# Kernel optimization log

Measured on AMD Instinct MI355X. Metric: run time of the kernel, lower is better.

## Reference

```python
import jax, jax.numpy as jnp
import numpy as np

B, C, H, W = 4, 512, 64, 64
R = 8
D = C // R  # inner channels = 64


def setup_inputs() -> dict:
    key = jax.random.key(0)
    k1, k2, k3 = jax.random.split(key, 3)
    x = jax.random.normal(k1, (B, C, H, W), dtype=jnp.float32)
    # 1x1 conv weights, stored as [out, in] (kernel spatial dims are 1)
    w_qkv = jax.random.normal(k2, (3 * D, C), dtype=jnp.float32) * (1.0 / np.sqrt(C))
    w_out = jax.random.normal(k3, (C, D), dtype=jnp.float32) * (1.0 / np.sqrt(D))
    # nn.Parameter(torch.zeros(1)) in the original; use nonzero so output != input
    scale = jnp.array([0.3], dtype=jnp.float32)
    return {"x": x, "w_qkv": w_qkv, "w_out": w_out, "scale": scale}


def reference(x, w_qkv, w_out, scale):
    b, c, h, w = x.shape
    hw = h * w
    # 1x1 conv == channel matmul
    t = jnp.einsum('oc,bchw->bohw', w_qkv, x)  # [B, 3D, H, W]
    d = t.shape[1] // 3
    key_ = t[:, :d].reshape(b, d, hw)      # chunk order: key, query, value
    query = t[:, d:2 * d].reshape(b, d, hw)
    value = t[:, 2 * d:].reshape(b, d, hw)
    # scores[b, k, q] = sum_d key[b,d,k] * query[b,d,q]
    scores = jnp.einsum('bdk,bdq->bkq', key_, query)  # [B, hw, hw]
    # NB: original uses Softmax(dim=1) -> normalize over the KEY axis
    attn = jax.nn.softmax(scores, axis=1)
    out = jnp.einsum('bdk,bkq->bdq', value, attn)     # [B, D, hw]
    out = out.reshape(b, d, h, w)
    out = jnp.einsum('oc,bchw->bohw', w_out, out)     # [B, C, H, W]
    return scale * out + x
```

## Files before the change

kernel.cpp:

```cpp
#include <hip/hip_runtime.h>
#include <hip/hip_bf16.h>
#include <string.h>

#define B_ 4
#define C_ 512
#define D_ 64
#define HW_ 4096
#define NCHUNK 4
#define KT_PER_CHUNK 16

typedef __attribute__((ext_vector_type(8))) short bf16x8;
typedef __attribute__((ext_vector_type(4))) float f32x4;

__device__ __forceinline__ unsigned short f2bf(float f) {
    unsigned int u = __builtin_bit_cast(unsigned int, f);
    u += 0x7fffu + ((u >> 16) & 1u);
    return (unsigned short)(u >> 16);
}

__device__ __forceinline__ unsigned int pack2bf(float lo, float hi) {
    __hip_bfloat162 h = __float22bfloat162_rn(float2{lo, hi});
    unsigned int r;
    memcpy(&r, &h, sizeof(r));
    return r;
}

#if __has_builtin(__builtin_amdgcn_exp2f)
#define EXP2(x) __builtin_amdgcn_exp2f(x)
#else
#define EXP2(x) __expf((x) * 0.6931471805599453f)
#endif

#define OFF_WQKV 0u
#define OFF_WOUT 196608u
#define OFF_PART 262144u
#define OFF_KT   17039360u
#define OFF_QT   19136512u
#define OFF_V    21233664u
#define OFF_ML   25427968u

__global__ __launch_bounds__(256) void k_convw(const float* __restrict__ wqkv,
                                               const float* __restrict__ wout,
                                               unsigned short* __restrict__ wq_b,
                                               unsigned short* __restrict__ wo_b) {
    int i = blockIdx.x * 256 + threadIdx.x;
    if (i < 192 * C_) wq_b[i] = f2bf(wqkv[i]);
    if (i < C_ * D_)  wo_b[i] = f2bf(wout[i]);
}

__global__ __launch_bounds__(256) void k_qkv(const float* __restrict__ x,
                                             const unsigned short* __restrict__ wq,
                                             unsigned short* __restrict__ kt,
                                             unsigned short* __restrict__ qt,
                                             unsigned short* __restrict__ v) {
    __shared__ float tile[64][33];
    __shared__ unsigned short xb[32][64];
    int pT = blockIdx.x, b = blockIdx.y;
    int tid = threadIdx.x, wid = tid >> 6, lane = tid & 63;
    int g = lane >> 4, r16 = lane & 15;
    int pp0 = pT * 32;
    int lp = tid & 31, lc = tid >> 5;
    int pl = tid >> 3, ch = tid & 7;

    float rx[8];
    auto gload = [&](int ct) {
        #pragma unroll
        for (int r = 0; r < 8; ++r)
            rx[r] = x[(size_t)(b * C_ + ct * 64 + lc * 8 + r) * HW_ + pp0 + lp];
    };

    f32x4 acc[3][2] = {};
    gload(0);
    for (int ct = 0; ct < 8; ++ct) {
        #pragma unroll
        for (int r = 0; r < 8; ++r) tile[lc * 8 + r][lp] = rx[r];
        __syncthreads();
        unsigned int pk[4];
        #pragma unroll
        for (int j = 0; j < 4; ++j)
            pk[j] = pack2bf(tile[ch * 8 + 2 * j][pl], tile[ch * 8 + 2 * j + 1][pl]);
        *(uint4*)(&xb[pl][0] + ((ch ^ (pl & 7)) << 3)) =
            make_uint4(pk[0], pk[1], pk[2], pk[3]);
        if (ct + 1 < 8) gload(ct + 1);
        __syncthreads();
        #pragma unroll
        for (int cs = 0; cs < 2; ++cs) {
            bf16x8 bb[2];
            #pragma unroll
            for (int ps = 0; ps < 2; ++ps) {
                int row = ps * 16 + r16;
                bb[ps] = *(const bf16x8*)(&xb[row][0] + (((cs * 4 + g) ^ (row & 7)) << 3));
            }
            #pragma unroll
            for (int ot = 0; ot < 3; ++ot) {
                bf16x8 a = *(const bf16x8*)(wq + (size_t)(wid * 48 + ot * 16 + r16) * C_
                                            + ct * 64 + cs * 32 + g * 8);
                #pragma unroll
                for (int ps = 0; ps < 2; ++ps)
                    acc[ot][ps] = __builtin_amdgcn_mfma_f32_16x16x32_bf16(a, bb[ps], acc[ot][ps], 0, 0, 0);
            }
        }
    }
    #pragma unroll
    for (int ot = 0; ot < 3; ++ot) {
        int obase = wid * 48 + ot * 16;
        int oT = obase >> 6;
        int dbase = (obase & 63) + 4 * g;
        #pragma unroll
        for (int ps = 0; ps < 2; ++ps) {
            int pp = pp0 + ps * 16 + r16;
            if (oT < 2) {
                unsigned short* dst = (oT == 0) ? kt : qt;
                float qs = (oT == 1) ? 1.4426950408889634f : 1.0f;
                unsigned int u0 = pack2bf(acc[ot][ps][0] * qs, acc[ot][ps][1] * qs);
                unsigned int u1 = pack2bf(acc[ot][ps][2] * qs, acc[ot][ps][3] * qs);
                *reinterpret_cast<uint2*>(dst + (size_t)(b * HW_ + pp) * D_ + dbase) =
                    make_uint2(u0, u1);
            } else {
                #pragma unroll
                for (int r = 0; r < 4; ++r)
                    v[(size_t)(b * D_ + dbase + r) * HW_ + pp] = f2bf(acc[ot][ps][r]);
            }
        }
    }
}

__global__ __launch_bounds__(256, 2) void k_attn(const unsigned short* __restrict__ kt,
                                                 const unsigned short* __restrict__ qt,
                                                 const unsigned short* __restrict__ v,
                                                 float* __restrict__ part,
                                                 float* __restrict__ ml) {
    __shared__ unsigned short klds[2][64][64];
    __shared__ unsigned short vlds[2][64][64];
    __shared__ unsigned short plds[4][32][64];
    int qT = blockIdx.x, chunk = blockIdx.y, b = blockIdx.z;
    int tid = threadIdx.x, wid = tid >> 6, lane = tid & 63;
    int g = lane >> 4, r16 = lane & 15;
    int q0 = qT * 128 + wid * 32;

    const unsigned short* qpA = qt + (size_t)(b * HW_ + q0 + r16) * D_ + g * 8;
    const unsigned short* qpB = qpA + (size_t)16 * D_;
    bf16x8 qf0A = *(const bf16x8*)(qpA);
    bf16x8 qf1A = *(const bf16x8*)(qpA + 32);
    bf16x8 qf0B = *(const bf16x8*)(qpB);
    bf16x8 qf1B = *(const bf16x8*)(qpB + 32);

    int isV = tid >> 7, tt = tid & 127;
    int srow = tt >> 1, shalf = tt & 1;
    const unsigned short* sbase = isV
        ? (v  + (size_t)b * D_ * HW_ + (size_t)srow * HW_ + shalf * 32)
        : (kt + (size_t)b * HW_ * D_ + (size_t)srow * D_  + shalf * 32);
    const int smul = isV ? 1 : D_;
    const int k0 = chunk * (KT_PER_CHUNK * 64);

    uint4 rr0, rr1, rr2, rr3;
    auto gload = [&](int t) {
        const uint4* s = (const uint4*)(sbase + (size_t)(k0 + t * 64) * smul);
        rr0 = s[0]; rr1 = s[1]; rr2 = s[2]; rr3 = s[3];
    };
    auto swrite = [&](int buf) {
        unsigned short* Lb = isV ? &vlds[buf][0][0] : &klds[buf][0][0];
        unsigned short* rowp = Lb + srow * 64;
        int swz = srow & 7, c0 = shalf * 4;
        *(uint4*)(rowp + (((c0 + 0) ^ swz) << 3)) = rr0;
        *(uint4*)(rowp + (((c0 + 1) ^ swz) << 3)) = rr1;
        *(uint4*)(rowp + (((c0 + 2) ^ swz) << 3)) = rr2;
        *(uint4*)(rowp + (((c0 + 3) ^ swz) << 3)) = rr3;
    };

    gload(0);
    swrite(0);
    gload(1);
    __syncthreads();

    f32x4 accA[4] = {}, accB[4] = {};
    float lsumA = 0.f, lsumB = 0.f;
    int cur = 0;
    unsigned short* pb = &plds[wid][0][0];

    for (int t = 0; t < KT_PER_CHUNK; ++t) {
        if (t + 1 < KT_PER_CHUNK) swrite(cur ^ 1);
        if (t + 2 < KT_PER_CHUNK) gload(t + 2);

        f32x4 sA[4], sB[4];
        #pragma unroll
        for (int ks = 0; ks < 4; ++ks) {
            int row = ks * 16 + r16;
            const unsigned short* rp = &klds[cur][0][0] + row * 64;
            int swz = row & 7;
            bf16x8 kf0 = *(const bf16x8*)(rp + ((g ^ swz) << 3));
            bf16x8 kf1 = *(const bf16x8*)(rp + (((g + 4) ^ swz) << 3));
            f32x4 za = {};
            za = __builtin_amdgcn_mfma_f32_16x16x32_bf16(kf0, qf0A, za, 0, 0, 0);
            za = __builtin_amdgcn_mfma_f32_16x16x32_bf16(kf1, qf1A, za, 0, 0, 0);
            sA[ks] = za;
            f32x4 zb = {};
            zb = __builtin_amdgcn_mfma_f32_16x16x32_bf16(kf0, qf0B, zb, 0, 0, 0);
            zb = __builtin_amdgcn_mfma_f32_16x16x32_bf16(kf1, qf1B, zb, 0, 0, 0);
            sB[ks] = zb;
        }
        float tsA = 0.f, tsB = 0.f;
        #pragma unroll
        for (int ks = 0; ks < 4; ++ks) {
            int ch = (2 * ks + (g >> 1)) ^ (r16 & 7);
            {
                float e0 = EXP2(sA[ks][0]);
                float e1 = EXP2(sA[ks][1]);
                float e2 = EXP2(sA[ks][2]);
                float e3 = EXP2(sA[ks][3]);
                tsA += (e0 + e1) + (e2 + e3);
                *(uint2*)(pb + r16 * 64 + (ch << 3) + 4 * (g & 1)) =
                    make_uint2(pack2bf(e0, e1), pack2bf(e2, e3));
            }
            {
                float e0 = EXP2(sB[ks][0]);
                float e1 = EXP2(sB[ks][1]);
                float e2 = EXP2(sB[ks][2]);
                float e3 = EXP2(sB[ks][3]);
                tsB += (e0 + e1) + (e2 + e3);
                *(uint2*)(pb + (r16 + 16) * 64 + (ch << 3) + 4 * (g & 1)) =
                    make_uint2(pack2bf(e0, e1), pack2bf(e2, e3));
            }
        }
        lsumA += tsA;
        lsumB += tsB;
        asm volatile("s_waitcnt lgkmcnt(0)" ::: "memory");
        int pswz = r16 & 7;
        bf16x8 pf0A = *(const bf16x8*)(pb + r16 * 64 + ((g ^ pswz) << 3));
        bf16x8 pf1A = *(const bf16x8*)(pb + r16 * 64 + (((g + 4) ^ pswz) << 3));
        bf16x8 pf0B = *(const bf16x8*)(pb + (r16 + 16) * 64 + ((g ^ pswz) << 3));
        bf16x8 pf1B = *(const bf16x8*)(pb + (r16 + 16) * 64 + (((g + 4) ^ pswz) << 3));
        #pragma unroll
        for (int dt = 0; dt < 4; ++dt) {
            int row = dt * 16 + r16;
            const unsigned short* rp = &vlds[cur][0][0] + row * 64;
            int swz = row & 7;
            bf16x8 vf0 = *(const bf16x8*)(rp + ((g ^ swz) << 3));
            bf16x8 vf1 = *(const bf16x8*)(rp + (((g + 4) ^ swz) << 3));
            accA[dt] = __builtin_amdgcn_mfma_f32_16x16x32_bf16(vf0, pf0A, accA[dt], 0, 0, 0);
            accA[dt] = __builtin_amdgcn_mfma_f32_16x16x32_bf16(vf1, pf1A, accA[dt], 0, 0, 0);
            accB[dt] = __builtin_amdgcn_mfma_f32_16x16x32_bf16(vf0, pf0B, accB[dt], 0, 0, 0);
            accB[dt] = __builtin_amdgcn_mfma_f32_16x16x32_bf16(vf1, pf1B, accB[dt], 0, 0, 0);
        }
        __syncthreads();
        cur ^= 1;
    }

    lsumA += __shfl_xor(lsumA, 16);
    lsumA += __shfl_xor(lsumA, 32);
    lsumB += __shfl_xor(lsumB, 16);
    lsumB += __shfl_xor(lsumB, 32);

    int rowA = ((b * NCHUNK + chunk) * HW_) + q0 + r16;
    int rowB = rowA + 16;
    #pragma unroll
    for (int dt = 0; dt < 4; ++dt) {
        *reinterpret_cast<f32x4*>(&part[(size_t)rowA * D_ + dt * 16 + 4 * g]) = accA[dt];
        *reinterpret_cast<f32x4*>(&part[(size_t)rowB * D_ + dt * 16 + 4 * g]) = accB[dt];
    }
    if (g == 0) {
        ml[2 * rowA]     = 0.0f;
        ml[2 * rowA + 1] = lsumA;
        ml[2 * rowB]     = 0.0f;
        ml[2 * rowB + 1] = lsumB;
    }
}

__global__ __launch_bounds__(256) void k_out(const unsigned short* __restrict__ wo,
                                             const float* __restrict__ part,
                                             const float* __restrict__ ml,
                                             const float* __restrict__ x,
                                             const float* __restrict__ scale,
                                             float* __restrict__ out) {
    __shared__ unsigned short alds[32][64];
    int pT = blockIdx.x, b = blockIdx.y;
    int tid = threadIdx.x;
    int pp0 = pT * 32;
    {
        int pl = tid >> 3, dgg = tid & 7;
        int q = pp0 + pl;
        float wi[NCHUNK];
        {
            float mi[NCHUNK], li[NCHUNK];
            #pragma unroll
            for (int i = 0; i < NCHUNK; ++i) {
                int row = (b * NCHUNK + i) * HW_ + q;
                mi[i] = ml[2 * row];
                li[i] = ml[2 * row + 1];
            }
            float M = mi[0];
            #pragma unroll
            for (int i = 1; i < NCHUNK; ++i) M = fmaxf(M, mi[i]);
            float L = 0.f;
            #pragma unroll
            for (int i = 0; i < NCHUNK; ++i) {
                wi[i] = EXP2(mi[i] - M);
                L += wi[i] * li[i];
            }
            float invL = 1.0f / L;
            #pragma unroll
            for (int i = 0; i < NCHUNK; ++i) wi[i] *= invL;
        }
        float o8[8] = {};
        #pragma unroll
        for (int i = 0; i < NCHUNK; ++i) {
            const float* pvp = &part[(size_t)((b * NCHUNK + i) * HW_ + q) * D_ + dgg * 8];
            f32x4 pv0 = *(const f32x4*)(pvp);
            f32x4 pv1 = *(const f32x4*)(pvp + 4);
            o8[0] += wi[i] * pv0[0]; o8[1] += wi[i] * pv0[1];
            o8[2] += wi[i] * pv0[2]; o8[3] += wi[i] * pv0[3];
            o8[4] += wi[i] * pv1[0]; o8[5] += wi[i] * pv1[1];
            o8[6] += wi[i] * pv1[2]; o8[7] += wi[i] * pv1[3];
        }
        unsigned int pk[4];
        #pragma unroll
        for (int j = 0; j < 4; ++j)
            pk[j] = pack2bf(o8[2 * j], o8[2 * j + 1]);
        *(uint4*)(&alds[pl][0] + ((dgg ^ (pl & 7)) << 3)) =
            make_uint4(pk[0], pk[1], pk[2], pk[3]);
    }
    __syncthreads();
    int wid = tid >> 6, lane = tid & 63;
    int g = lane >> 4, r16 = lane & 15;
    float sc = scale[0];
    bf16x8 bfr[2][2];
    #pragma unroll
    for (int ps = 0; ps < 2; ++ps) {
        int row = ps * 16 + r16;
        const unsigned short* rp = &alds[row][0];
        int swz = row & 7;
        bfr[ps][0] = *(const bf16x8*)(rp + (((0 * 4 + g) ^ swz) << 3));
        bfr[ps][1] = *(const bf16x8*)(rp + (((1 * 4 + g) ^ swz) << 3));
    }
    #pragma unroll 2
    for (int ot = 0; ot < 8; ++ot) {
        int orow = wid * 128 + ot * 16;
        bf16x8 a0 = *(const bf16x8*)(wo + (size_t)(orow + r16) * D_ + g * 8);
        bf16x8 a1 = *(const bf16x8*)(wo + (size_t)(orow + r16) * D_ + 32 + g * 8);
        #pragma unroll
        for (int ps = 0; ps < 2; ++ps) {
            f32x4 acc = {};
            acc = __builtin_amdgcn_mfma_f32_16x16x32_bf16(a0, bfr[ps][0], acc, 0, 0, 0);
            acc = __builtin_amdgcn_mfma_f32_16x16x32_bf16(a1, bfr[ps][1], acc, 0, 0, 0);
            int o = orow + 4 * g;
            int pp = pp0 + ps * 16 + r16;
            size_t base = (size_t)(b * C_ + o) * HW_ + pp;
            #pragma unroll
            for (int r = 0; r < 4; ++r)
                out[base + (size_t)r * HW_] = sc * acc[r] + x[base + (size_t)r * HW_];
        }
    }
}

extern "C" void kernel_launch(void* const* d_in, const int* in_sizes, int n_in,
                              void* d_out, int out_size, void* d_ws, size_t ws_size,
                              hipStream_t stream) {
    const float* x     = (const float*)d_in[0];
    const float* wqkv  = (const float*)d_in[1];
    const float* wout  = (const float*)d_in[2];
    const float* scale = (const float*)d_in[3];
    char* ws = (char*)d_ws;
    unsigned short* wq_b = (unsigned short*)(ws + OFF_WQKV);
    unsigned short* wo_b = (unsigned short*)(ws + OFF_WOUT);
    float*          prt  = (float*)(ws + OFF_PART);
    unsigned short* ktb  = (unsigned short*)(ws + OFF_KT);
    unsigned short* qtb  = (unsigned short*)(ws + OFF_QT);
    unsigned short* vb   = (unsigned short*)(ws + OFF_V);
    float*          mlb  = (float*)(ws + OFF_ML);

    hipLaunchKernelGGL(k_convw, dim3(384), dim3(256), 0, stream, wqkv, wout, wq_b, wo_b);
    hipLaunchKernelGGL(k_qkv,   dim3(128, 4),   dim3(256), 0, stream, x, wq_b, ktb, qtb, vb);
    hipLaunchKernelGGL(k_attn,  dim3(32, NCHUNK, 4), dim3(256), 0, stream, ktb, qtb, vb, prt, mlb);
    hipLaunchKernelGGL(k_out,   dim3(128, 4),   dim3(256), 0, stream, wo_b, prt, mlb, x, scale,
                       (float*)d_out);
}
```

Baseline: 76.86 us.

## Stage K/V tiles with direct global-to-LDS loads instead of register staging

Replaces the register-staged K/V tile loads (global to VGPR, then swizzled ds_write) with global_load_lds async copies that write straight into a merged double-buffered LDS array. The swizzle moves to the global source addresses so the LDS layout stays the same, and prefetch depth drops from two tiles ahead to one. The aim is to cut VGPR pressure and the ds_write instructions in the attention loop. The risk is that a single tile of lookahead may expose global latency, and correctness depends on the waitcnt/barrier covering the async LDS writes.

After: 78.98 us. 2.8% more time.

```diff
diff --git a/kernel.cpp b/kernel.cpp
--- a/kernel.cpp
+++ b/kernel.cpp
@@ -130,13 +130,13 @@
                                                  const unsigned short* __restrict__ v,
                                                  float* __restrict__ part,
                                                  float* __restrict__ ml) {
-    __shared__ unsigned short klds[2][64][64];
-    __shared__ unsigned short vlds[2][64][64];
+    __shared__ unsigned short kv[2][2][64][64];
     __shared__ unsigned short plds[4][32][64];
     int qT = blockIdx.x, chunk = blockIdx.y, b = blockIdx.z;
     int tid = threadIdx.x, wid = tid >> 6, lane = tid & 63;
     int g = lane >> 4, r16 = lane & 15;
     int q0 = qT * 128 + wid * 32;
+    const int k0 = chunk * (KT_PER_CHUNK * 64);
 
     const unsigned short* qpA = qt + (size_t)(b * HW_ + q0 + r16) * D_ + g * 8;
     const unsigned short* qpB = qpA + (size_t)16 * D_;
@@ -145,32 +145,38 @@
     bf16x8 qf0B = *(const bf16x8*)(qpB);
     bf16x8 qf1B = *(const bf16x8*)(qpB + 32);
 
-    int isV = tid >> 7, tt = tid & 127;
-    int srow = tt >> 1, shalf = tt & 1;
-    const unsigned short* sbase = isV
-        ? (v  + (size_t)b * D_ * HW_ + (size_t)srow * HW_ + shalf * 32)
-        : (kt + (size_t)b * HW_ * D_ + (size_t)srow * D_  + shalf * 32);
-    const int smul = isV ? 1 : D_;
-    const int k0 = chunk * (KT_PER_CHUNK * 64);
-
-    uint4 rr0, rr1, rr2, rr3;
-    auto gload = [&](int t) {
-        const uint4* s = (const uint4*)(sbase + (size_t)(k0 + t * 64) * smul);
-        rr0 = s[0]; rr1 = s[1]; rr2 = s[2]; rr3 = s[3];
+    const unsigned short* gsrc[4];
+    size_t gstep[4];
+    unsigned int lofs[4];
+    #pragma unroll
+    for (int i = 0; i < 4; ++i) {
+        int L = (wid << 12) + (i << 10) + (lane << 4);
+        int which = L >> 13;
+        int row   = (L >> 7) & 63;
+        int clin  = (L >> 4) & 7;
+        int gch   = clin ^ (row & 7);
+        if (which == 0) {
+            gsrc[i]  = kt + (size_t)(b * HW_ + k0 + row) * D_ + gch * 8;
+            gstep[i] = (size_t)64 * D_;
+        } else {
+            gsrc[i]  = v + (size_t)(b * D_ + row) * HW_ + k0 + gch * 8;
+            gstep[i] = 64;
+        }
+        lofs[i] = (unsigned)((wid << 11) + (i << 9));
+    }
+    unsigned short* kvbase = &kv[0][0][0][0];
+    auto stage = [&](int t, int buf) {
+        #pragma unroll
+        for (int i = 0; i < 4; ++i) {
+            const unsigned short* gp = gsrc[i] + (size_t)t * gstep[i];
+            unsigned short* lp = kvbase + buf * 8192 + lofs[i];
+            __builtin_amdgcn_global_load_lds(
+                (const __attribute__((address_space(1))) unsigned int*)gp,
+                (__attribute__((address_space(3))) unsigned int*)lp, 16, 0, 0);
+        }
     };
-    auto swrite = [&](int buf) {
-        unsigned short* Lb = isV ? &vlds[buf][0][0] : &klds[buf][0][0];
-        unsigned short* rowp = Lb + srow * 64;
-        int swz = srow & 7, c0 = shalf * 4;
-        *(uint4*)(rowp + (((c0 + 0) ^ swz) << 3)) = rr0;
-        *(uint4*)(rowp + (((c0 + 1) ^ swz) << 3)) = rr1;
-        *(uint4*)(rowp + (((c0 + 2) ^ swz) << 3)) = rr2;
-        *(uint4*)(rowp + (((c0 + 3) ^ swz) << 3)) = rr3;
-    };
-
-    gload(0);
-    swrite(0);
-    gload(1);
+
+    stage(0, 0);
     __syncthreads();
 
     f32x4 accA[4] = {}, accB[4] = {};
@@ -179,14 +185,13 @@
     unsigned short* pb = &plds[wid][0][0];
 
     for (int t = 0; t < KT_PER_CHUNK; ++t) {
-        if (t + 1 < KT_PER_CHUNK) swrite(cur ^ 1);
-        if (t + 2 < KT_PER_CHUNK) gload(t + 2);
+        if (t + 1 < KT_PER_CHUNK) stage(t + 1, cur ^ 1);
 
         f32x4 sA[4], sB[4];
         #pragma unroll
         for (int ks = 0; ks < 4; ++ks) {
             int row = ks * 16 + r16;
-            const unsigned short* rp = &klds[cur][0][0] + row * 64;
+            const unsigned short* rp = &kv[cur][0][row][0];
             int swz = row & 7;
             bf16x8 kf0 = *(const bf16x8*)(rp + ((g ^ swz) << 3));
             bf16x8 kf1 = *(const bf16x8*)(rp + (((g + 4) ^ swz) << 3));
@@ -233,7 +238,7 @@
         #pragma unroll
         for (int dt = 0; dt < 4; ++dt) {
             int row = dt * 16 + r16;
-            const unsigned short* rp = &vlds[cur][0][0] + row * 64;
+            const unsigned short* rp = &kv[cur][1][row][0];
             int swz = row & 7;
             bf16x8 vf0 = *(const bf16x8*)(rp + ((g ^ swz) << 3));
             bf16x8 vf1 = *(const bf16x8*)(rp + (((g + 4) ^ swz) << 3));
```

## Keep softmax probabilities in registers using 16x16x16 MFMA for PV

Applied to the files above, without the earlier changes.

Removes the per-wave LDS round trip for the exponentiated scores by feeding them straight from the QK^T accumulator layout into 16x16x16 bf16 MFMAs for the P*V product. This eliminates the LDS stores, the lgkmcnt wait and the reloads of P. It frees 16KB of shared memory per block. The trade-off is twice as many MFMA instructions, each at half the K-depth, plus narrower 8-byte V reads from LDS.

New measurement: 78.26 us. Within noise of the previous version (+1.8%).

```diff
diff --git a/kernel.cpp b/kernel.cpp
--- a/kernel.cpp
+++ b/kernel.cpp
@@ -10,6 +10,7 @@
 #define KT_PER_CHUNK 16
 
 typedef __attribute__((ext_vector_type(8))) short bf16x8;
+typedef __attribute__((ext_vector_type(4))) short bf16x4;
 typedef __attribute__((ext_vector_type(4))) float f32x4;
 
 __device__ __forceinline__ unsigned short f2bf(float f) {
@@ -23,6 +24,11 @@
     unsigned int r;
     memcpy(&r, &h, sizeof(r));
     return r;
+}
+
+__device__ __forceinline__ bf16x4 mk4(unsigned int u0, unsigned int u1) {
+    unsigned long long ull = (unsigned long long)u0 | ((unsigned long long)u1 << 32);
+    return __builtin_bit_cast(bf16x4, ull);
 }
 
 #if __has_builtin(__builtin_amdgcn_exp2f)
@@ -132,7 +138,6 @@
                                                  float* __restrict__ ml) {
     __shared__ unsigned short klds[2][64][64];
     __shared__ unsigned short vlds[2][64][64];
-    __shared__ unsigned short plds[4][32][64];
     int qT = blockIdx.x, chunk = blockIdx.y, b = blockIdx.z;
     int tid = threadIdx.x, wid = tid >> 6, lane = tid & 63;
     int g = lane >> 4, r16 = lane & 15;
@@ -176,7 +181,6 @@
     f32x4 accA[4] = {}, accB[4] = {};
     float lsumA = 0.f, lsumB = 0.f;
     int cur = 0;
-    unsigned short* pb = &plds[wid][0][0];
 
     for (int t = 0; t < KT_PER_CHUNK; ++t) {
         if (t + 1 < KT_PER_CHUNK) swrite(cur ^ 1);
@@ -200,17 +204,16 @@
             sB[ks] = zb;
         }
         float tsA = 0.f, tsB = 0.f;
+        bf16x4 pA[4], pB[4];
         #pragma unroll
         for (int ks = 0; ks < 4; ++ks) {
-            int ch = (2 * ks + (g >> 1)) ^ (r16 & 7);
             {
                 float e0 = EXP2(sA[ks][0]);
                 float e1 = EXP2(sA[ks][1]);
                 float e2 = EXP2(sA[ks][2]);
                 float e3 = EXP2(sA[ks][3]);
                 tsA += (e0 + e1) + (e2 + e3);
-                *(uint2*)(pb + r16 * 64 + (ch << 3) + 4 * (g & 1)) =
-                    make_uint2(pack2bf(e0, e1), pack2bf(e2, e3));
+                pA[ks] = mk4(pack2bf(e0, e1), pack2bf(e2, e3));
             }
             {
                 float e0 = EXP2(sB[ks][0]);
@@ -218,29 +221,23 @@
                 float e2 = EXP2(sB[ks][2]);
                 float e3 = EXP2(sB[ks][3]);
                 tsB += (e0 + e1) + (e2 + e3);
-                *(uint2*)(pb + (r16 + 16) * 64 + (ch << 3) + 4 * (g & 1)) =
-                    make_uint2(pack2bf(e0, e1), pack2bf(e2, e3));
+                pB[ks] = mk4(pack2bf(e0, e1), pack2bf(e2, e3));
             }
         }
         lsumA += tsA;
         lsumB += tsB;
-        asm volatile("s_waitcnt lgkmcnt(0)" ::: "memory");
-        int pswz = r16 & 7;
-        bf16x8 pf0A = *(const bf16x8*)(pb + r16 * 64 + ((g ^ pswz) << 3));
-        bf16x8 pf1A = *(const bf16x8*)(pb + r16 * 64 + (((g + 4) ^ pswz) << 3));
-        bf16x8 pf0B = *(const bf16x8*)(pb + (r16 + 16) * 64 + ((g ^ pswz) << 3));
-        bf16x8 pf1B = *(const bf16x8*)(pb + (r16 + 16) * 64 + (((g + 4) ^ pswz) << 3));
         #pragma unroll
         for (int dt = 0; dt < 4; ++dt) {
             int row = dt * 16 + r16;
             const unsigned short* rp = &vlds[cur][0][0] + row * 64;
             int swz = row & 7;
-            bf16x8 vf0 = *(const bf16x8*)(rp + ((g ^ swz) << 3));
-            bf16x8 vf1 = *(const bf16x8*)(rp + (((g + 4) ^ swz) << 3));
-            accA[dt] = __builtin_amdgcn_mfma_f32_16x16x32_bf16(vf0, pf0A, accA[dt], 0, 0, 0);
-            accA[dt] = __builtin_amdgcn_mfma_f32_16x16x32_bf16(vf1, pf1A, accA[dt], 0, 0, 0);
-            accB[dt] = __builtin_amdgcn_mfma_f32_16x16x32_bf16(vf0, pf0B, accB[dt], 0, 0, 0);
-            accB[dt] = __builtin_amdgcn_mfma_f32_16x16x32_bf16(vf1, pf1B, accB[dt], 0, 0, 0);
+            #pragma unroll
+            for (int ks = 0; ks < 4; ++ks) {
+                int c = 2 * ks + (g >> 1);
+                bf16x4 vf = *(const bf16x4*)(rp + ((c ^ swz) << 3) + 4 * (g & 1));
+                accA[dt] = __builtin_amdgcn_mfma_f32_16x16x16bf16_1k(vf, pA[ks], accA[dt], 0, 0, 0);
+                accB[dt] = __builtin_amdgcn_mfma_f32_16x16x16bf16_1k(vf, pB[ks], accB[dt], 0, 0, 0);
+            }
         }
         __syncthreads();
         cur ^= 1;
```
